# Performance work log

Measured on AMD Instinct MI355X. Metric: run time of the kernel, lower is better.

Reference implementation:

```python
import jax, jax.numpy as jnp
import numpy as np
import math

NUM_HEADS = 16
ROPE_BASE = 10000.0


def _rope_cos_sin(seq_len, head_dim, dtype):
    # Qwen2-style rotary embeddings. The torch source builds cos/sin of width
    # head_dim by concatenating freqs with itself, so the first and second
    # halves are identical; the half-width table below is the equivalent math.
    half = head_dim // 2
    inv_freq = 1.0 / (ROPE_BASE ** (jnp.arange(0, head_dim, 2, dtype=jnp.float32) / head_dim))
    t = jnp.arange(seq_len, dtype=jnp.float32)
    freqs = jnp.einsum('i,j->ij', t, inv_freq)  # [S, half]
    cos = jnp.cos(freqs).astype(dtype)[None, None]  # [1,1,S,half]
    sin = jnp.sin(freqs).astype(dtype)[None, None]
    return cos, sin


def _apply_rope(x, cos, sin):
    # x: [B, H, S, D]; split-half rotation (Qwen2 rotate-half convention)
    half = x.shape[-1] // 2
    x1, x2 = x[..., :half], x[..., half:]
    return jnp.concatenate([x1 * cos - x2 * sin, x2 * cos + x1 * sin], axis=-1)


def setup_inputs() -> dict:
    key = jax.random.key(0)
    ks = jax.random.split(key, 5)
    B, S, H = 2, 2048, 2048
    scale = 1.0 / math.sqrt(H)
    return {
        'hidden_states': jax.random.normal(ks[0], (B, S, H), dtype=jnp.float32),
        'Wq': jax.random.normal(ks[1], (H, H), dtype=jnp.float32) * scale,
        'Wk': jax.random.normal(ks[2], (H, H), dtype=jnp.float32) * scale,
        'Wv': jax.random.normal(ks[3], (H, H), dtype=jnp.float32) * scale,
        'Wo': jax.random.normal(ks[4], (H, H), dtype=jnp.float32) * scale,
    }


def reference(hidden_states, Wq, Wk, Wv, Wo):
    B, S, H = hidden_states.shape
    nh = NUM_HEADS
    hd = H // nh

    def proj(W):
        # nn.Linear: x @ W.T ; then [B,S,H] -> [B,nh,S,hd]
        y = jnp.einsum('bsh,oh->bso', hidden_states, W)
        return y.reshape(B, S, nh, hd).transpose(0, 2, 1, 3)

    q, k, v = proj(Wq), proj(Wk), proj(Wv)

    cos, sin = _rope_cos_sin(S, hd, hidden_states.dtype)
    q = _apply_rope(q, cos, sin)
    k = _apply_rope(k, cos, sin)

    scores = jnp.einsum('bhqd,bhkd->bhqk', q, k) / math.sqrt(hd)
    causal = jnp.triu(jnp.full((S, S), -jnp.inf, dtype=scores.dtype), k=1)
    scores = scores + causal[None, None]
    probs = jax.nn.softmax(scores, axis=-1)

    ctx = jnp.einsum('bhqk,bhkd->bhqd', probs, v)  # [B,nh,S,hd]
    ctx = ctx.transpose(0, 2, 1, 3).reshape(B, S, H)
    out = jnp.einsum('bsh,oh->bso', ctx, Wo)
    return out
```

## Files before the change

kernel.cpp:

```cpp
#include <hip/hip_runtime.h>

#define S_LEN 2048
#define HID   2048
#define NHEAD 16
#define HD    128
#define BSZ   2
#define BS_TOT (BSZ * S_LEN)

typedef __bf16 bf16x8 __attribute__((ext_vector_type(8)));
typedef unsigned short u16x8 __attribute__((ext_vector_type(8)));
typedef unsigned short u16x4 __attribute__((ext_vector_type(4)));
typedef float f32x4 __attribute__((ext_vector_type(4)));

static __device__ __forceinline__ bf16x8 as_bf(u16x8 v) { return __builtin_bit_cast(bf16x8, v); }

static __device__ __forceinline__ unsigned short f2bf(float f) {
  __bf16 h = (__bf16)f;
  return __builtin_bit_cast(unsigned short, h);
}
static __device__ __forceinline__ float bf2f(unsigned short b) {
  unsigned int u = ((unsigned int)b) << 16;
  return __builtin_bit_cast(float, u);
}

static __device__ __forceinline__ void gload_lds16(const unsigned short* g, unsigned short* l) {
  __builtin_amdgcn_global_load_lds((const __attribute__((address_space(1))) unsigned int*)g,
                                   (__attribute__((address_space(3))) unsigned int*)l, 16, 0, 0);
}

__global__ __launch_bounds__(256) void cvt_bf16(const float* __restrict__ in,
                                                unsigned short* __restrict__ out) {
  int i = blockIdx.x * 256 + threadIdx.x;
  float4 v = ((const float4*)in)[i];
  ushort4 o;
  o.x = f2bf(v.x); o.y = f2bf(v.y); o.z = f2bf(v.z); o.w = f2bf(v.w);
  ((ushort4*)out)[i] = o;
}

__global__ __launch_bounds__(256) void rope_table(float* __restrict__ ct, float* __restrict__ st) {
  int id = blockIdx.x * 256 + threadIdx.x;
  int t = id >> 6, d = id & 63;
  float inv = powf(10000.0f, -(float)d * (1.0f / 64.0f));
  float f = (float)t * inv;
  float sv, cv;
  sincosf(f, &sv, &cv);
  ct[id] = cv; st[id] = sv;
}

__global__ __launch_bounds__(256) void rope_apply(unsigned short* __restrict__ q,
                                                  unsigned short* __restrict__ k,
                                                  const float* __restrict__ ct,
                                                  const float* __restrict__ st) {
  int id = blockIdx.x * 256 + threadIdx.x;
  int d = id & 63;
  int h = (id >> 6) & (NHEAD - 1);
  int m = id >> 10;
  int s = m & (S_LEN - 1);
  float c = ct[s * 64 + d], sn = st[s * 64 + d];
  size_t base = (size_t)m * HID + h * HD + d;
  float q1 = bf2f(q[base]), q2 = bf2f(q[base + 64]);
  q[base]      = f2bf(q1 * c - q2 * sn);
  q[base + 64] = f2bf(q2 * c + q1 * sn);
  float k1 = bf2f(k[base]), k2 = bf2f(k[base + 64]);
  k[base]      = f2bf(k1 * c - k2 * sn);
  k[base + 64] = f2bf(k2 * c + k1 * sn);
}

template <typename OutT>
__global__ __launch_bounds__(256) void gemm_bt(const unsigned short* __restrict__ A,
                                               const unsigned short* __restrict__ Bw,
                                               OutT* __restrict__ C, int M, int N, int K) {
  __shared__ __align__(16) unsigned short As[2][128 * 32];
  __shared__ __align__(16) unsigned short Bs[2][128 * 32];
  int x = (int)blockIdx.x;
  int x2 = (x & 7) * 64 + (x >> 3);
  const int nbn = N >> 7;
  int bm = x2 / nbn, bn = x2 % nbn;
  int tid = (int)threadIdx.x;
  int l = tid & 63, lr = l & 15, lg = l >> 4;
  int w = tid >> 6, wm = w >> 1, wn = w & 1;

  int w32 = 32 * w;
  int srow = w32 + (l >> 2);
  const unsigned short* gA = A + (size_t)(bm * 128 + srow) * K + (l & 3) * 8;
  const unsigned short* gB = Bw + (size_t)(bn * 128 + srow) * K + (l & 3) * 8;

  int aoff[4], boff[4];
#pragma unroll
  for (int i = 0; i < 4; ++i) {
    aoff[i] = (wm * 64 + i * 16 + lr) * 32 + lg * 8;
    boff[i] = (wn * 64 + i * 16 + lr) * 32 + lg * 8;
  }

  f32x4 zero = {0.f, 0.f, 0.f, 0.f};
  f32x4 acc[4][4];
#pragma unroll
  for (int mi = 0; mi < 4; ++mi)
#pragma unroll
    for (int ni = 0; ni < 4; ++ni) acc[mi][ni] = zero;

  int nk = K >> 5;

#define STAGE(buf, kt)                                                        \
  do {                                                                        \
    const unsigned short* pa_ = gA + (size_t)(kt) * 32;                       \
    const unsigned short* pb_ = gB + (size_t)(kt) * 32;                       \
    gload_lds16(pa_, &As[buf][w32 * 32]);                                     \
    gload_lds16(pa_ + (size_t)16 * K, &As[buf][(w32 + 16) * 32]);             \
    gload_lds16(pb_, &Bs[buf][w32 * 32]);                                     \
    gload_lds16(pb_ + (size_t)16 * K, &Bs[buf][(w32 + 16) * 32]);             \
  } while (0)

#define COMPUTE(buf)                                                          \
  do {                                                                        \
    u16x8 af[4], bfr[4];                                                      \
    _Pragma("unroll") for (int i = 0; i < 4; ++i) {                           \
      af[i] = *(const u16x8*)&As[buf][aoff[i]];                               \
      bfr[i] = *(const u16x8*)&Bs[buf][boff[i]];                              \
    }                                                                         \
    _Pragma("unroll") for (int mi = 0; mi < 4; ++mi)                          \
        _Pragma("unroll") for (int ni = 0; ni < 4; ++ni)                      \
            acc[mi][ni] = __builtin_amdgcn_mfma_f32_16x16x32_bf16(            \
                as_bf(af[mi]), as_bf(bfr[ni]), acc[mi][ni], 0, 0, 0);         \
  } while (0)

  STAGE(0, 0);
  __syncthreads();
  for (int kt = 0; kt < nk; kt += 2) {
    STAGE(1, kt + 1);
    COMPUTE(0);
    __syncthreads();
    if (kt + 2 < nk) STAGE(0, kt + 2);
    COMPUTE(1);
    __syncthreads();
  }
#undef STAGE
#undef COMPUTE

#pragma unroll
  for (int mi = 0; mi < 4; ++mi) {
#pragma unroll
    for (int ni = 0; ni < 4; ++ni) {
      int col = bn * 128 + wn * 64 + ni * 16 + lr;
#pragma unroll
      for (int j = 0; j < 4; ++j) {
        int rowm = bm * 128 + wm * 64 + mi * 16 + 4 * lg + j;
        float v = acc[mi][ni][j];
        if constexpr (sizeof(OutT) == 2) C[(size_t)rowm * N + col] = f2bf(v);
        else                             C[(size_t)rowm * N + col] = v;
      }
    }
  }
  (void)M;
}

__global__ __launch_bounds__(256, 2) void attn_fwd(const unsigned short* __restrict__ qg,
                                                   const unsigned short* __restrict__ kg,
                                                   const unsigned short* __restrict__ vt,
                                                   unsigned short* __restrict__ ctx) {
  __shared__ __align__(16) unsigned short Ks[64 * 128];
  __shared__ __align__(16) unsigned short Vs[128 * 64];
  __shared__ __align__(16) unsigned short Ps[4 * 32 * 64];

  int x = (int)blockIdx.x;
  int bh, qt;
  if (x < 256) { bh = x & 31;         qt = 15 - (x >> 5); }
  else         { bh = (x - 256) & 31; qt = (x - 256) >> 5; }
  int b = bh >> 4, h = bh & 15;
  int q0 = qt * 128;
  int nt = 2 * qt + 2;

  int tid = (int)threadIdx.x;
  int w = tid >> 6, l = tid & 63, lr = l & 15, lg = l >> 4;
  const float CEXP = 0.12751744f;
  const float THRRAW = 90.509668f;
  const int bS = b * S_LEN, h128 = h * HD;
  const int qw = q0 + w * 32;

  u16x8 qfr[2][4];
#pragma unroll
  for (int qf = 0; qf < 2; ++qf) {
    const unsigned short* qb = qg + (size_t)(bS + qw + qf * 16 + lr) * HID + h128;
#pragma unroll
    for (int kk = 0; kk < 4; ++kk) qfr[qf][kk] = *(const u16x8*)(qb + kk * 32 + lg * 8);
  }

  f32x4 zero = {0.f, 0.f, 0.f, 0.f};
  f32x4 oacc[2][8];
#pragma unroll
  for (int qf = 0; qf < 2; ++qf)
#pragma unroll
    for (int nj = 0; nj < 8; ++nj) oacc[qf][nj] = zero;
  float mrow[2] = {-1e30f, -1e30f}, lsum[2] = {0.f, 0.f};

  int rK[4], cK[4], dV[4], cV[4];
#pragma unroll
  for (int p = 0; p < 4; ++p) {
    int id = tid + p * 256;
    rK[p] = id >> 4; cK[p] = id & 15;
    dV[p] = id >> 3; cV[p] = id & 7;
  }

  u16x8 ka[4], va[4];
#pragma unroll
  for (int p = 0; p < 4; ++p) {
    ka[p] = *(const u16x8*)(kg + (size_t)(bS + rK[p]) * HID + h128 + cK[p] * 8);
    va[p] = *(const u16x8*)(vt + (size_t)(h128 + dV[p]) * BS_TOT + bS + cV[p] * 8);
  }

  for (int t = 0; t < nt; ++t) {
    int k0 = t * 64;
    __syncthreads();
#pragma unroll
    for (int p = 0; p < 4; ++p) {
      *(u16x8*)&Ks[rK[p] * 128 + ((cK[p] ^ (rK[p] & 15)) * 8)] = ka[p];
      *(u16x8*)&Vs[dV[p] * 64 + ((cV[p] ^ (dV[p] & 7)) * 8)] = va[p];
    }
    __syncthreads();
    if (t + 1 < nt) {
      int k1 = k0 + 64;
#pragma unroll
      for (int p = 0; p < 4; ++p) {
        ka[p] = *(const u16x8*)(kg + (size_t)(bS + k1 + rK[p]) * HID + h128 + cK[p] * 8);
        va[p] = *(const u16x8*)(vt + (size_t)(h128 + dV[p]) * BS_TOT + bS + k1 + cV[p] * 8);
      }
    }

    if (k0 <= qw + 31) {
      f32x4 sac[2][4];
#pragma unroll
      for (int qf = 0; qf < 2; ++qf)
#pragma unroll
        for (int ni = 0; ni < 4; ++ni) sac[qf][ni] = zero;
#pragma unroll
      for (int kk = 0; kk < 4; ++kk) {
#pragma unroll
        for (int ni = 0; ni < 4; ++ni) {
          u16x8 kf = *(const u16x8*)&Ks[(ni * 16 + lr) * 128 + (((kk * 4 + lg) ^ lr) * 8)];
          sac[0][ni] = __builtin_amdgcn_mfma_f32_16x16x32_bf16(as_bf(kf), as_bf(qfr[0][kk]), sac[0][ni], 0, 0, 0);
          sac[1][ni] = __builtin_amdgcn_mfma_f32_16x16x32_bf16(as_bf(kf), as_bf(qfr[1][kk]), sac[1][ni], 0, 0, 0);
        }
      }
      bool needmask = (k0 + 63 > qw);

#pragma unroll
      for (int qf = 0; qf < 2; ++qf) {
        float s[4][4];
#pragma unroll
        for (int ni = 0; ni < 4; ++ni)
#pragma unroll
          for (int j = 0; j < 4; ++j) s[ni][j] = sac[qf][ni][j];
        if (needmask) {
          int qgl = qw + qf * 16 + lr;
#pragma unroll
          for (int ni = 0; ni < 4; ++ni)
#pragma unroll
            for (int j = 0; j < 4; ++j)
              if (k0 + ni * 16 + 4 * lg + j > qgl) s[ni][j] = -1e30f;
        }
        float mx = s[0][0];
#pragma unroll
        for (int ni = 0; ni < 4; ++ni)
#pragma unroll
          for (int j = 0; j < 4; ++j) mx = fmaxf(mx, s[ni][j]);
        mx = fmaxf(mx, __shfl_xor(mx, 16));
        mx = fmaxf(mx, __shfl_xor(mx, 32));
        if (!__all(mx - mrow[qf] <= THRRAW)) {
          float mn = fmaxf(mrow[qf], mx);
          float al = exp2f((mrow[qf] - mn) * CEXP);
          mrow[qf] = mn;
          lsum[qf] *= al;
          float a0 = __shfl(al, 4 * lg + 0, 16);
          float a1 = __shfl(al, 4 * lg + 1, 16);
          float a2 = __shfl(al, 4 * lg + 2, 16);
          float a3 = __shfl(al, 4 * lg + 3, 16);
#pragma unroll
          for (int nj = 0; nj < 8; ++nj) {
            oacc[qf][nj][0] *= a0; oacc[qf][nj][1] *= a1;
            oacc[qf][nj][2] *= a2; oacc[qf][nj][3] *= a3;
          }
        }
        float m = mrow[qf];
        float rs = 0.f;
#pragma unroll
        for (int ni = 0; ni < 4; ++ni)
#pragma unroll
          for (int j = 0; j < 4; ++j) {
            float p = exp2f((s[ni][j] - m) * CEXP);
            s[ni][j] = p; rs += p;
          }
        lsum[qf] += rs;
        unsigned short* pw = &Ps[w * 2048];
#pragma unroll
        for (int ni = 0; ni < 4; ++ni) {
          u16x4 pv = {f2bf(s[ni][0]), f2bf(s[ni][1]), f2bf(s[ni][2]), f2bf(s[ni][3])};
          *(u16x4*)&pw[(qf * 16 + lr) * 64 + (((2 * ni + (lg >> 1)) ^ (lr & 7)) * 8) + (lg & 1) * 4] = pv;
        }
      }

      const unsigned short* pw = &Ps[w * 2048];
#pragma unroll
      for (int kk2 = 0; kk2 < 2; ++kk2) {
        u16x8 pa0 = *(const u16x8*)&pw[(0 * 16 + lr) * 64 + (((kk2 * 4 + lg) ^ (lr & 7)) * 8)];
        u16x8 pa1 = *(const u16x8*)&pw[(1 * 16 + lr) * 64 + (((kk2 * 4 + lg) ^ (lr & 7)) * 8)];
#pragma unroll
        for (int nj = 0; nj < 8; ++nj) {
          u16x8 vf = *(const u16x8*)&Vs[(nj * 16 + lr) * 64 + (((kk2 * 4 + lg) ^ (lr & 7)) * 8)];
          oacc[0][nj] = __builtin_amdgcn_mfma_f32_16x16x32_bf16(as_bf(pa0), as_bf(vf), oacc[0][nj], 0, 0, 0);
          oacc[1][nj] = __builtin_amdgcn_mfma_f32_16x16x32_bf16(as_bf(pa1), as_bf(vf), oacc[1][nj], 0, 0, 0);
        }
      }
    }
  }

#pragma unroll
  for (int qf = 0; qf < 2; ++qf) {
    float ls = lsum[qf];
    ls += __shfl_xor(ls, 16);
    ls += __shfl_xor(ls, 32);
    float rl = 1.0f / ls;
    float r0 = __shfl(rl, 4 * lg + 0, 16);
    float r1 = __shfl(rl, 4 * lg + 1, 16);
    float r2 = __shfl(rl, 4 * lg + 2, 16);
    float r3 = __shfl(rl, 4 * lg + 3, 16);
    size_t obase = (size_t)(bS + qw + qf * 16 + 4 * lg) * HID + h128;
#pragma unroll
    for (int nj = 0; nj < 8; ++nj) {
      ctx[obase + 0 * HID + nj * 16 + lr] = f2bf(oacc[qf][nj][0] * r0);
      ctx[obase + 1 * HID + nj * 16 + lr] = f2bf(oacc[qf][nj][1] * r1);
      ctx[obase + 2 * HID + nj * 16 + lr] = f2bf(oacc[qf][nj][2] * r2);
      ctx[obase + 3 * HID + nj * 16 + lr] = f2bf(oacc[qf][nj][3] * r3);
    }
  }
}

extern "C" void kernel_launch(void* const* d_in, const int* in_sizes, int n_in,
                              void* d_out, int out_size, void* d_ws, size_t ws_size,
                              hipStream_t stream) {
  const float* hs = (const float*)d_in[0];
  const float* Wq = (const float*)d_in[1];
  const float* Wk = (const float*)d_in[2];
  const float* Wv = (const float*)d_in[3];
  const float* Wo = (const float*)d_in[4];

  char* ws = (char*)d_ws;
  unsigned short* hsb = (unsigned short*)(ws);
  unsigned short* wqb = (unsigned short*)(ws + 16777216);
  unsigned short* wkb = (unsigned short*)(ws + 25165824);
  unsigned short* wvb = (unsigned short*)(ws + 33554432);
  unsigned short* wob = (unsigned short*)(ws + 41943040);
  unsigned short* qb  = (unsigned short*)(ws + 50331648);
  unsigned short* kb  = (unsigned short*)(ws + 67108864);
  unsigned short* vtb = (unsigned short*)(ws + 83886080);
  float* ctab = (float*)(ws + 100663296);
  float* stab = (float*)(ws + 101187584);
  unsigned short* ctxb = hsb;

  cvt_bf16<<<8192, 256, 0, stream>>>(hs, hsb);
  cvt_bf16<<<4096, 256, 0, stream>>>(Wq, wqb);
  cvt_bf16<<<4096, 256, 0, stream>>>(Wk, wkb);
  cvt_bf16<<<4096, 256, 0, stream>>>(Wv, wvb);
  cvt_bf16<<<4096, 256, 0, stream>>>(Wo, wob);
  rope_table<<<512, 256, 0, stream>>>(ctab, stab);

  gemm_bt<unsigned short><<<512, 256, 0, stream>>>(hsb, wqb, qb, BS_TOT, HID, HID);
  gemm_bt<unsigned short><<<512, 256, 0, stream>>>(hsb, wkb, kb, BS_TOT, HID, HID);
  gemm_bt<unsigned short><<<512, 256, 0, stream>>>(wvb, hsb, vtb, HID, BS_TOT, HID);

  rope_apply<<<16384, 256, 0, stream>>>(qb, kb, ctab, stab);

  attn_fwd<<<512, 256, 0, stream>>>(qb, kb, vtb, ctxb);

  gemm_bt<float><<<512, 256, 0, stream>>>(ctxb, wob, (float*)d_out, BS_TOT, HID, HID);

  (void)in_sizes; (void)n_in; (void)out_size; (void)ws_size;
}
```

Baseline: 314.7 us.

## Deepen GEMM LDS pipeline to four stages with swizzle; halve attention block size

The GEMM moves from a double-buffered LDS loop to a four-buffer ring that keeps three tiles in flight. It uses explicit vmcnt waits and one barrier per k-step, plus an XOR swizzle on LDS stores and reads to reduce bank conflicts. Attention blocks drop from 256 to 128 threads and 64 query rows, with twice as many blocks and a reworked heavy-first causal ordering. The aim is to hide global load latency and improve load balance and occupancy, at the cost of more LDS per GEMM block, fragile hand-written waitcnt counts, and reloading each K/V tile for every 64 query rows.

```diff
diff --git a/kernel.cpp b/kernel.cpp
--- a/kernel.cpp
+++ b/kernel.cpp
@@ -70,8 +70,8 @@
 __global__ __launch_bounds__(256) void gemm_bt(const unsigned short* __restrict__ A,
                                                const unsigned short* __restrict__ Bw,
                                                OutT* __restrict__ C, int M, int N, int K) {
-  __shared__ __align__(16) unsigned short As[2][128 * 32];
-  __shared__ __align__(16) unsigned short Bs[2][128 * 32];
+  __shared__ __align__(16) unsigned short As[4][128 * 32];
+  __shared__ __align__(16) unsigned short Bs[4][128 * 32];
   int x = (int)blockIdx.x;
   int x2 = (x & 7) * 64 + (x >> 3);
   const int nbn = N >> 7;
@@ -82,14 +82,16 @@
 
   int w32 = 32 * w;
   int srow = w32 + (l >> 2);
-  const unsigned short* gA = A + (size_t)(bm * 128 + srow) * K + (l & 3) * 8;
-  const unsigned short* gB = Bw + (size_t)(bn * 128 + srow) * K + (l & 3) * 8;
-
+  int ssw = ((l >> 2) ^ (l >> 4)) & 3;
+  const unsigned short* gA = A + (size_t)(bm * 128 + srow) * K + (((l & 3) ^ ssw) << 3);
+  const unsigned short* gB = Bw + (size_t)(bn * 128 + srow) * K + (((l & 3) ^ ssw) << 3);
+
+  int rsw = (lr ^ (lr >> 2)) & 3;
   int aoff[4], boff[4];
 #pragma unroll
   for (int i = 0; i < 4; ++i) {
-    aoff[i] = (wm * 64 + i * 16 + lr) * 32 + lg * 8;
-    boff[i] = (wn * 64 + i * 16 + lr) * 32 + lg * 8;
+    aoff[i] = (wm * 64 + i * 16 + lr) * 32 + ((lg ^ rsw) << 3);
+    boff[i] = (wn * 64 + i * 16 + lr) * 32 + ((lg ^ rsw) << 3);
   }
 
   f32x4 zero = {0.f, 0.f, 0.f, 0.f};
@@ -125,14 +127,16 @@
   } while (0)
 
   STAGE(0, 0);
-  __syncthreads();
-  for (int kt = 0; kt < nk; kt += 2) {
-    STAGE(1, kt + 1);
-    COMPUTE(0);
-    __syncthreads();
-    if (kt + 2 < nk) STAGE(0, kt + 2);
-    COMPUTE(1);
-    __syncthreads();
+  STAGE(1, 1);
+  STAGE(2, 2);
+  asm volatile("s_waitcnt vmcnt(8)" ::: "memory");
+  __builtin_amdgcn_s_barrier();
+#pragma unroll 4
+  for (int kt = 0; kt < nk; ++kt) {
+    COMPUTE(kt & 3);
+    asm volatile("s_waitcnt vmcnt(4) lgkmcnt(0)" ::: "memory");
+    __builtin_amdgcn_s_barrier();
+    STAGE((kt + 3) & 3, (kt + 3) & (nk - 1));
   }
 #undef STAGE
 #undef COMPUTE
@@ -154,21 +158,20 @@
   (void)M;
 }
 
-__global__ __launch_bounds__(256, 2) void attn_fwd(const unsigned short* __restrict__ qg,
+__global__ __launch_bounds__(128, 2) void attn_fwd(const unsigned short* __restrict__ qg,
                                                    const unsigned short* __restrict__ kg,
                                                    const unsigned short* __restrict__ vt,
                                                    unsigned short* __restrict__ ctx) {
   __shared__ __align__(16) unsigned short Ks[64 * 128];
   __shared__ __align__(16) unsigned short Vs[128 * 64];
-  __shared__ __align__(16) unsigned short Ps[4 * 32 * 64];
-
-  int x = (int)blockIdx.x;
-  int bh, qt;
-  if (x < 256) { bh = x & 31;         qt = 15 - (x >> 5); }
-  else         { bh = (x - 256) & 31; qt = (x - 256) >> 5; }
+  __shared__ __align__(16) unsigned short Ps[2 * 32 * 64];
+
+  int i = (int)blockIdx.x;
+  int rank = i >> 5, bh = i & 31;
+  int qt = (rank < 16) ? (31 - rank) : (rank - 16);
   int b = bh >> 4, h = bh & 15;
-  int q0 = qt * 128;
-  int nt = 2 * qt + 2;
+  int q0 = qt * 64;
+  int nt = qt + 1;
 
   int tid = (int)threadIdx.x;
   int w = tid >> 6, l = tid & 63, lr = l & 15, lg = l >> 4;
@@ -193,17 +196,17 @@
     for (int nj = 0; nj < 8; ++nj) oacc[qf][nj] = zero;
   float mrow[2] = {-1e30f, -1e30f}, lsum[2] = {0.f, 0.f};
 
-  int rK[4], cK[4], dV[4], cV[4];
-#pragma unroll
-  for (int p = 0; p < 4; ++p) {
-    int id = tid + p * 256;
+  int rK[8], cK[8], dV[8], cV[8];
+#pragma unroll
+  for (int p = 0; p < 8; ++p) {
+    int id = tid + p * 128;
     rK[p] = id >> 4; cK[p] = id & 15;
     dV[p] = id >> 3; cV[p] = id & 7;
   }
 
-  u16x8 ka[4], va[4];
-#pragma unroll
-  for (int p = 0; p < 4; ++p) {
+  u16x8 ka[8], va[8];
+#pragma unroll
+  for (int p = 0; p < 8; ++p) {
     ka[p] = *(const u16x8*)(kg + (size_t)(bS + rK[p]) * HID + h128 + cK[p] * 8);
     va[p] = *(const u16x8*)(vt + (size_t)(h128 + dV[p]) * BS_TOT + bS + cV[p] * 8);
   }
@@ -212,7 +215,7 @@
     int k0 = t * 64;
     __syncthreads();
 #pragma unroll
-    for (int p = 0; p < 4; ++p) {
+    for (int p = 0; p < 8; ++p) {
       *(u16x8*)&Ks[rK[p] * 128 + ((cK[p] ^ (rK[p] & 15)) * 8)] = ka[p];
       *(u16x8*)&Vs[dV[p] * 64 + ((cV[p] ^ (dV[p] & 7)) * 8)] = va[p];
     }
@@ -220,7 +223,7 @@
     if (t + 1 < nt) {
       int k1 = k0 + 64;
 #pragma unroll
-      for (int p = 0; p < 4; ++p) {
+      for (int p = 0; p < 8; ++p) {
         ka[p] = *(const u16x8*)(kg + (size_t)(bS + k1 + rK[p]) * HID + h128 + cK[p] * 8);
         va[p] = *(const u16x8*)(vt + (size_t)(h128 + dV[p]) * BS_TOT + bS + k1 + cV[p] * 8);
       }
@@ -369,7 +372,7 @@
 
   rope_apply<<<16384, 256, 0, stream>>>(qb, kb, ctab, stab);
 
-  attn_fwd<<<512, 256, 0, stream>>>(qb, kb, vtb, ctxb);
+  attn_fwd<<<1024, 128, 0, stream>>>(qb, kb, vtb, ctxb);
 
   gemm_bt<float><<<512, 256, 0, stream>>>(ctxb, wob, (float*)d_out, BS_TOT, HID, HID);
 
```

Result: slower. 461.4 us (+46.6%).
